# Performance work log

Measured on AMD Instinct MI355X. Metric: run time of the kernel, lower is better.

The kernel has to match this reference:

```python
import jax, jax.numpy as jnp
import numpy as np

N_HEAD = 16
D_HEAD = 64
D_LATENT = 32
BLOCK_SIZE = 2048


def rope_cache(dim, max_seq_len, theta=10000.0):
    inv_freq = 1.0 / (theta ** (jnp.arange(0, dim, 2, dtype=jnp.float32) / dim))
    t = jnp.arange(max_seq_len, dtype=jnp.float32)
    freqs = jnp.einsum('i,j->ij', t, inv_freq)        # [T, dim/2]
    emb = jnp.concatenate([freqs, freqs], axis=-1)    # [T, dim]
    return jnp.cos(emb), jnp.sin(emb)


def apply_rope(x, cos, sin):
    # x: [B, H, T, C]; interleaved-pair rotation as in the torch module
    B, H, T, C = x.shape
    c = cos[:T][None, None]
    s = sin[:T][None, None]
    x1 = x[..., 0::2]
    x2 = x[..., 1::2]
    rotated = jnp.stack((-x2, x1), axis=-1).reshape(B, H, T, C)
    return x * c + rotated * s


def setup_inputs() -> dict:
    key = jax.random.key(0)
    ks = jax.random.split(key, 7)
    sd = 0.02
    return {
        'x':   jax.random.normal(ks[0], (2, 2048, 1024), dtype=jnp.float32),
        'Wq':  jax.random.normal(ks[1], (1024, 1024), dtype=jnp.float32) * sd,
        'Wk':  jax.random.normal(ks[2], (512, 1024), dtype=jnp.float32) * sd,
        'Wv':  jax.random.normal(ks[3], (512, 1024), dtype=jnp.float32) * sd,
        'Wku': jax.random.normal(ks[4], (64, 32), dtype=jnp.float32) * sd,
        'Wvu': jax.random.normal(ks[5], (64, 32), dtype=jnp.float32) * sd,
        'Wc':  jax.random.normal(ks[6], (1024, 1024), dtype=jnp.float32) * sd,
    }


def reference(x, Wq, Wk, Wv, Wku, Wvu, Wc):
    B, T, C = x.shape
    H, Dh, Dl = N_HEAD, D_HEAD, D_LATENT

    # latent KV (compressed cache entries)
    k_lat = (x @ Wk.T).reshape(B, T, H, Dl)   # [B,T,H,Dl]
    v_lat = (x @ Wv.T).reshape(B, T, H, Dl)

    # q and up-projected k/v -> [B,H,T,Dh]
    q = (x @ Wq.T).reshape(B, T, H, Dh).transpose(0, 2, 1, 3)
    k = jnp.einsum('bthl,dl->bhtd', k_lat, Wku)
    v = jnp.einsum('bthl,dl->bhtd', v_lat, Wvu)

    cos, sin = rope_cache(Dh, BLOCK_SIZE)
    q = apply_rope(q, cos, sin)
    k = apply_rope(k, cos, sin)

    scale = 1.0 / jnp.sqrt(jnp.asarray(Dh, dtype=x.dtype))
    att = jnp.einsum('bhqd,bhkd->bhqk', q, k) * scale   # [B,H,T,T]
    causal = jnp.tril(jnp.ones((T, T), dtype=bool))
    att = jnp.where(causal[None, None], att, -jnp.inf)
    att = jax.nn.softmax(att, axis=-1)

    y = jnp.einsum('bhqk,bhkd->bhqd', att, v)           # [B,H,T,Dh]
    y = y.transpose(0, 2, 1, 3).reshape(B, T, C) @ Wc.T  # [B,T,C]
    return y, k_lat, v_lat
```

## Files before the change

### kernel.cpp

```cpp
#include <hip/hip_runtime.h>
#include <math.h>

#define NHEAD  16
#define DHEAD  64
#define DLAT   32
#define TSEQ   2048
#define NBATCH 2
#define CDIM   1024
#define MROWS  (NBATCH*TSEQ)

typedef __attribute__((ext_vector_type(8))) short bf16x8;
typedef __attribute__((ext_vector_type(4))) float f32x4;

#define AS1 __attribute__((address_space(1)))
#define AS3 __attribute__((address_space(3)))

__device__ __forceinline__ unsigned short f2bf(float f) {
    union { float f; unsigned u; } v; v.f = f;
    unsigned r = v.u + 0x7fff + ((v.u >> 16) & 1);
    return (unsigned short)(r >> 16);
}

__device__ __forceinline__ unsigned pk2(float lo, float hi) {
    return (unsigned)f2bf(lo) | ((unsigned)f2bf(hi) << 16);
}

__device__ __forceinline__ unsigned pack_trunc(float hi, float lo) {
    return __builtin_amdgcn_perm(__float_as_uint(hi), __float_as_uint(lo), 0x07060302u);
}

__device__ __forceinline__ void gld_lds16(const unsigned short* g, unsigned short* l) {
    __builtin_amdgcn_global_load_lds((const AS1 void*)g, (AS3 void*)l, 16, 0, 0);
}

__global__ __launch_bounds__(256) void cvt_all(
        const float* __restrict__ x,  const float* __restrict__ wq,
        const float* __restrict__ wk, const float* __restrict__ wv,
        const float* __restrict__ wc, const float* __restrict__ wku,
        const float* __restrict__ wvu,
        unsigned short* __restrict__ xb, unsigned short* __restrict__ wall) {
    int i = (blockIdx.x * 256 + threadIdx.x) * 4;
    const float* src; unsigned short* dst; int off;
    if      (i < 4194304) { src = x;   dst = xb;             off = 0;       }
    else if (i < 5242880) { src = wq;  dst = wall;           off = 4194304; }
    else if (i < 5767168) { src = wk;  dst = wall + 1048576; off = 5242880; }
    else if (i < 6291456) { src = wv;  dst = wall + 1572864; off = 5767168; }
    else if (i < 7340032) { src = wc;  dst = wall + 2097152; off = 6291456; }
    else if (i < 7342080) { src = wku; dst = wall + 3145728; off = 7340032; }
    else                  { src = wvu; dst = wall + 3147776; off = 7342080; }
    float4 v = *(const float4*)(src + (i - off));
    ushort4 o = { f2bf(v.x), f2bf(v.y), f2bf(v.z), f2bf(v.w) };
    *(ushort4*)(dst + (i - off)) = o;
}

__device__ __forceinline__ void gemm_core(
        const unsigned short* __restrict__ A, const unsigned short* __restrict__ W,
        int K, int bm, int bn, unsigned short* As, unsigned short* Bs,
        f32x4 (&acc)[4][4]) {
    const int tid = threadIdx.x;
    const int w = tid >> 6, lane = tid & 63;
    const int quad = lane >> 4, l16 = lane & 15;
    const int wm = (w >> 1) * 64, wn = (w & 1) * 64;

    const int lr = lane >> 2;
    const int le = (lane & 3) * 8;
    const unsigned short* Ag0 = A + (size_t)(bm + w*32 + lr) * K + le;
    const unsigned short* Wg0 = W + (size_t)(bn + w*32 + lr) * K + le;
    unsigned short* AsD0 = &As[(w*32 +  0) * 32];
    unsigned short* AsD1 = &As[(w*32 + 16) * 32];
    unsigned short* BsD0 = &Bs[(w*32 +  0) * 32];
    unsigned short* BsD1 = &Bs[(w*32 + 16) * 32];

    for (int k0 = 0; k0 < K; k0 += 32) {
        gld_lds16(Ag0 + k0,                AsD0);
        gld_lds16(Ag0 + k0 + (size_t)16*K, AsD1);
        gld_lds16(Wg0 + k0,                BsD0);
        gld_lds16(Wg0 + k0 + (size_t)16*K, BsD1);
        __syncthreads();
        bf16x8 af[4], bf[4];
        #pragma unroll
        for (int t = 0; t < 4; ++t)
            af[t] = *(const bf16x8*)&As[(wm + t*16 + l16)*32 + quad*8];
        #pragma unroll
        for (int c = 0; c < 4; ++c)
            bf[c] = *(const bf16x8*)&Bs[(wn + c*16 + l16)*32 + quad*8];
        #pragma unroll
        for (int t = 0; t < 4; ++t)
            #pragma unroll
            for (int c = 0; c < 4; ++c)
                acc[t][c] = __builtin_amdgcn_mfma_f32_16x16x32_bf16(af[t], bf[c], acc[t][c], 0, 0, 0);
        __syncthreads();
    }
}

__global__ __launch_bounds__(256) void gemm_proj(
        const unsigned short* __restrict__ A, const unsigned short* __restrict__ W,
        float* __restrict__ qproj, float* __restrict__ okl, float* __restrict__ ovl,
        int K) {
    __shared__ unsigned short As[128*32];
    __shared__ unsigned short Bs[128*32];
    const int bm = blockIdx.y * 128, bn = blockIdx.x * 128;
    f32x4 acc[4][4] = {};
    gemm_core(A, W, K, bm, bn, As, Bs, acc);

    const int tid = threadIdx.x;
    const int w = tid >> 6, lane = tid & 63;
    const int quad = lane >> 4, l16 = lane & 15;
    const int wm = (w >> 1) * 64, wn = (w & 1) * 64;

    float* base; int ldo;
    if (bn < 1024)      { base = qproj + bn;        ldo = 1024; }
    else if (bn < 1536) { base = okl + (bn - 1024); ldo = 512;  }
    else                { base = ovl + (bn - 1536); ldo = 512;  }

    #pragma unroll
    for (int t = 0; t < 4; ++t)
        #pragma unroll
        for (int c = 0; c < 4; ++c)
            #pragma unroll
            for (int r = 0; r < 4; ++r) {
                int row = bm + wm + t*16 + quad*4 + r;
                int col = wn + c*16 + l16;
                base[(size_t)row * ldo + col] = acc[t][c][r];
            }
}

__global__ __launch_bounds__(256) void gemm_out(
        const unsigned short* __restrict__ A, const unsigned short* __restrict__ W,
        float* __restrict__ O, int N, int K) {
    __shared__ unsigned short As[128*32];
    __shared__ unsigned short Bs[128*32];
    const int bm = blockIdx.y * 128, bn = blockIdx.x * 128;
    f32x4 acc[4][4] = {};
    gemm_core(A, W, K, bm, bn, As, Bs, acc);

    const int tid = threadIdx.x;
    const int w = tid >> 6, lane = tid & 63;
    const int quad = lane >> 4, l16 = lane & 15;
    const int wm = (w >> 1) * 64, wn = (w & 1) * 64;
    #pragma unroll
    for (int t = 0; t < 4; ++t)
        #pragma unroll
        for (int c = 0; c < 4; ++c)
            #pragma unroll
            for (int r = 0; r < 4; ++r) {
                int row = bm + wm + t*16 + quad*4 + r;
                int col = bn + wn + c*16 + l16;
                O[(size_t)row * N + col] = acc[t][c][r];
            }
}

__global__ __launch_bounds__(256) void latup(
        const float* __restrict__ qproj, const float* __restrict__ klat,
        const float* __restrict__ vlat,
        const unsigned short* __restrict__ wkub, const unsigned short* __restrict__ wvub,
        unsigned short* __restrict__ qb, unsigned short* __restrict__ kb,
        unsigned short* __restrict__ vt) {
    __shared__ __attribute__((aligned(16))) unsigned short ksh[4][16][72];
    __shared__ __attribute__((aligned(16))) unsigned short qsh[4][16][72];
    __shared__ __attribute__((aligned(16))) unsigned short vsh[4][64][24];

    const int bh = blockIdx.y, b = bh >> 4, h = bh & 15;
    const int tid = threadIdx.x, w = tid >> 6, lane = tid & 63;
    const int quad = lane >> 4, l16 = lane & 15;
    const int tw = blockIdx.x * 64 + w * 16;
    const int t  = tw + l16;

    const float* klp = klat + ((size_t)(b*TSEQ + t))*(NHEAD*DLAT) + h*DLAT + quad*8;
    const float* vlp = vlat + ((size_t)(b*TSEQ + t))*(NHEAD*DLAT) + h*DLAT + quad*8;
    float4 kA = *(const float4*)klp, kB = *(const float4*)(klp + 4);
    float4 vA = *(const float4*)vlp, vB = *(const float4*)(vlp + 4);

    bf16x8 xk[4], xv[4];
    #pragma unroll
    for (int c = 0; c < 4; ++c) {
        xk[c] = *(const bf16x8*)&wkub[(c*16 + l16)*DLAT + quad*8];
        xv[c] = *(const bf16x8*)&wvub[(c*16 + l16)*DLAT + quad*8];
    }

    union { bf16x8 v; unsigned u[4]; } yk, yv;
    yk.u[0] = pk2(kA.x, kA.y); yk.u[1] = pk2(kA.z, kA.w);
    yk.u[2] = pk2(kB.x, kB.y); yk.u[3] = pk2(kB.z, kB.w);
    yv.u[0] = pk2(vA.x, vA.y); yv.u[1] = pk2(vA.z, vA.w);
    yv.u[2] = pk2(vB.x, vB.y); yv.u[3] = pk2(vB.z, vB.w);

    f32x4 aK[4], aV[4];
    #pragma unroll
    for (int c = 0; c < 4; ++c) {
        f32x4 z = {0.f, 0.f, 0.f, 0.f};
        aK[c] = __builtin_amdgcn_mfma_f32_16x16x32_bf16(xk[c], yk.v, z, 0, 0, 0);
        aV[c] = __builtin_amdgcn_mfma_f32_16x16x32_bf16(xv[c], yv.v, z, 0, 0, 0);
    }

    float C0[4], S0[4], C1[4], S1[4];
    const float tf = (float)t;
    #pragma unroll
    for (int j = 0; j < 4; ++j) {
        float f0 = (float)(quad*4 + j);
        __sincosf(tf * __expf(-f0 * 0.28782313662425572f),          &S0[j], &C0[j]);
        __sincosf(tf * __expf(-(f0 + 16.f) * 0.28782313662425572f), &S1[j], &C1[j]);
    }

    const float* qrow = qproj + ((size_t)(b*TSEQ + t))*CDIM + h*DHEAD;
    #pragma unroll
    for (int c = 0; c < 4; ++c) {
        const float* Cs = (c & 1) ? C1 : C0;
        const float* Ss = (c & 1) ? S1 : S0;
        float a0 = aK[c][0], a1 = aK[c][1], a2 = aK[c][2], a3 = aK[c][3];
        unsigned kw0 = pk2(a0*Cs[0] - a1*Ss[0], a1*Cs[1] + a0*Ss[1]);
        unsigned kw1 = pk2(a2*Cs[2] - a3*Ss[2], a3*Cs[3] + a2*Ss[3]);
        *(uint2*)&ksh[w][l16][c*16 + quad*4] = make_uint2(kw0, kw1);

        float4 qv = *(const float4*)(qrow + c*16 + quad*4);
        unsigned qw0 = pk2((qv.x*Cs[0] - qv.y*Ss[0])*0.125f, (qv.y*Cs[1] + qv.x*Ss[1])*0.125f);
        unsigned qw1 = pk2((qv.z*Cs[2] - qv.w*Ss[2])*0.125f, (qv.w*Cs[3] + qv.z*Ss[3])*0.125f);
        *(uint2*)&qsh[w][l16][c*16 + quad*4] = make_uint2(qw0, qw1);

        vsh[w][c*16 + quad*4 + 0][l16] = f2bf(aV[c][0]);
        vsh[w][c*16 + quad*4 + 1][l16] = f2bf(aV[c][1]);
        vsh[w][c*16 + quad*4 + 2][l16] = f2bf(aV[c][2]);
        vsh[w][c*16 + quad*4 + 3][l16] = f2bf(aV[c][3]);
    }

    __asm__ __volatile__("s_waitcnt lgkmcnt(0)" ::: "memory");

    const int ro = lane >> 2, co = (lane & 3) * 16;
    size_t go = ((size_t)bh*TSEQ + tw + ro)*DHEAD + co;
    int4 k0o = *(const int4*)&ksh[w][ro][co];
    int4 k1o = *(const int4*)&ksh[w][ro][co + 8];
    *(int4*)&kb[go]     = k0o;
    *(int4*)&kb[go + 8] = k1o;
    int4 q0o = *(const int4*)&qsh[w][ro][co];
    int4 q1o = *(const int4*)&qsh[w][ro][co + 8];
    *(int4*)&qb[go]     = q0o;
    *(int4*)&qb[go + 8] = q1o;

    size_t vo = ((size_t)bh*DHEAD + lane)*TSEQ + tw;
    int4 v0o = *(const int4*)&vsh[w][lane][0];
    int4 v1o = *(const int4*)&vsh[w][lane][8];
    *(int4*)&vt[vo]     = v0o;
    *(int4*)&vt[vo + 8] = v1o;
}

__global__ __launch_bounds__(256, 2) void flash_attn(
        const unsigned short* __restrict__ qb, const unsigned short* __restrict__ kb,
        const unsigned short* __restrict__ vtb, unsigned short* __restrict__ yatt) {
    const int bh = blockIdx.x;
    const int b = bh >> 4, h = bh & 15;

    __shared__ unsigned short Ks[2][128][64];
    __shared__ unsigned short VTs[2][64][128];

    const int tid  = threadIdx.x;
    const int wq   = tid >> 6;
    const int lane = tid & 63;
    const int quad = lane >> 4;
    const int l16  = lane & 15;

    const unsigned short* Kbase = kb  + (size_t)bh * TSEQ * DHEAD;
    const unsigned short* Vbase = vtb + (size_t)bh * DHEAD * TSEQ;

    const int kr8 = lane >> 3, kcp = lane & 7;
    const int kcl = (kcp ^ kr8) * 8;
    const int vr4 = lane >> 4, vcp = lane & 15;

    const int kx0 = (quad ^ (l16 & 7)) * 8;
    const int kx1 = ((quad + 4) ^ (l16 & 7)) * 8;

    const int idx01 = (((lane >> 4) & 1) * 32 + l16) * 4;
    const int idx23 = idx01 + 64;
    const bool hi = (lane & 32) != 0;

    for (int half = 0; half < 2; ++half) {
        const int qt = half ? (31 - (int)blockIdx.y) : (int)blockIdx.y;
        const int n128 = (qt + 2) >> 1;

        const unsigned short* qbase =
            qb + ((size_t)bh*TSEQ + qt*64 + wq*16 + l16) * DHEAD + quad*8;
        bf16x8 qB0 = *(const bf16x8*)qbase;
        bf16x8 qB1 = *(const bf16x8*)(qbase + 32);

        f32x4 oacc[4] = {};
        float m_run = -1e30f, l_run = 0.f;

        __syncthreads();
        #pragma unroll
        for (int i = 0; i < 4; ++i) {
            gld_lds16(Kbase + (size_t)(wq*32 + i*8 + kr8)*DHEAD + kcl,
                      &Ks[0][wq*32 + i*8][0]);
            int vcl = (vcp ^ ((i*4 + vr4) & 15)) * 8;
            gld_lds16(Vbase + (size_t)(wq*16 + i*4 + vr4)*TSEQ + vcl,
                      &VTs[0][wq*16 + i*4][0]);
        }
        __syncthreads();

        for (int j = 0; j < n128; ++j) {
            const int buf = j & 1;
            if (j + 1 < n128) {
                const int kc = (j + 1) * 128;
                #pragma unroll
                for (int i = 0; i < 4; ++i) {
                    gld_lds16(Kbase + (size_t)(kc + wq*32 + i*8 + kr8)*DHEAD + kcl,
                              &Ks[buf^1][wq*32 + i*8][0]);
                    int vcl = (vcp ^ ((i*4 + vr4) & 15)) * 8;
                    gld_lds16(Vbase + (size_t)(wq*16 + i*4 + vr4)*TSEQ + kc + vcl,
                              &VTs[buf^1][wq*16 + i*4][0]);
                }
            }

            f32x4 sacc[8];
            #pragma unroll
            for (int c = 0; c < 8; ++c) {
                bf16x8 ak0 = *(const bf16x8*)&Ks[buf][c*16 + l16][kx0];
                bf16x8 ak1 = *(const bf16x8*)&Ks[buf][c*16 + l16][kx1];
                f32x4 z = {0.f, 0.f, 0.f, 0.f};
                z = __builtin_amdgcn_mfma_f32_16x16x32_bf16(ak0, qB0, z, 0, 0, 0);
                z = __builtin_amdgcn_mfma_f32_16x16x32_bf16(ak1, qB1, z, 0, 0, 0);
                sacc[c] = z;
            }
            if (j == n128 - 1) {
                #pragma unroll
                for (int c = 0; c < 8; ++c)
                    #pragma unroll
                    for (int r = 0; r < 4; ++r)
                        if (j*128 + c*16 + quad*4 + r > qt*64 + wq*16 + l16)
                            sacc[c][r] = -1e30f;
            }

            float mx = -1e30f;
            #pragma unroll
            for (int c = 0; c < 8; ++c)
                #pragma unroll
                for (int r = 0; r < 4; ++r) mx = fmaxf(mx, sacc[c][r]);
            mx = fmaxf(mx, __shfl_xor(mx, 16, 64));
            mx = fmaxf(mx, __shfl_xor(mx, 32, 64));
            float mn = fmaxf(m_run, mx);
            float alpha = __expf(m_run - mn);
            m_run = mn;
            float ls = 0.f;
            #pragma unroll
            for (int c = 0; c < 8; ++c)
                #pragma unroll
                for (int r = 0; r < 4; ++r) {
                    float p = __expf(sacc[c][r] - mn);
                    sacc[c][r] = p;
                    ls += p;
                }
            ls += __shfl_xor(ls, 16, 64);
            ls += __shfl_xor(ls, 32, 64);
            l_run = l_run * alpha + ls;
            #pragma unroll
            for (int c = 0; c < 4; ++c)
                #pragma unroll
                for (int r = 0; r < 4; ++r) oacc[c][r] *= alpha;

            #pragma unroll
            for (int g = 0; g < 4; ++g) {
                unsigned p0a = pack_trunc(sacc[2*g][1],   sacc[2*g][0]);
                unsigned p0b = pack_trunc(sacc[2*g][3],   sacc[2*g][2]);
                unsigned p1a = pack_trunc(sacc[2*g+1][1], sacc[2*g+1][0]);
                unsigned p1b = pack_trunc(sacc[2*g+1][3], sacc[2*g+1][2]);
                union { bf16x8 v; int d[4]; } bP;
                int a0 = __builtin_amdgcn_ds_bpermute(idx01, (int)p0a);
                int b0 = __builtin_amdgcn_ds_bpermute(idx01, (int)p1a);
                bP.d[0] = hi ? b0 : a0;
                int a1 = __builtin_amdgcn_ds_bpermute(idx01, (int)p0b);
                int b1 = __builtin_amdgcn_ds_bpermute(idx01, (int)p1b);
                bP.d[1] = hi ? b1 : a1;
                int a2 = __builtin_amdgcn_ds_bpermute(idx23, (int)p0a);
                int b2 = __builtin_amdgcn_ds_bpermute(idx23, (int)p1a);
                bP.d[2] = hi ? b2 : a2;
                int a3 = __builtin_amdgcn_ds_bpermute(idx23, (int)p0b);
                int b3 = __builtin_amdgcn_ds_bpermute(idx23, (int)p1b);
                bP.d[3] = hi ? b3 : a3;
                #pragma unroll
                for (int c = 0; c < 4; ++c) {
                    bf16x8 av = *(const bf16x8*)&VTs[buf][c*16 + l16][((g*4 + quad) ^ l16) * 8];
                    oacc[c] = __builtin_amdgcn_mfma_f32_16x16x32_bf16(av, bP.v, oacc[c], 0, 0, 0);
                }
            }

            __syncthreads();
        }

        float invl = 1.0f / l_run;
        unsigned short* Wt = &Ks[0][0][0] + wq * (16*72);
        #pragma unroll
        for (int c = 0; c < 4; ++c)
            #pragma unroll
            for (int r = 0; r < 4; ++r)
                Wt[(size_t)l16*72 + c*16 + quad*4 + r] = f2bf(oacc[c][r] * invl);
        __asm__ __volatile__("" ::: "memory");
        #pragma unroll
        for (int p = 0; p < 2; ++p) {
            int row = p*8 + (lane >> 3);
            int d0 = (lane & 7) * 8;
            int4 val = *(const int4*)&Wt[row*72 + d0];
            int tg = qt*64 + wq*16 + row;
            *(int4*)&yatt[((size_t)(b*TSEQ + tg))*CDIM + h*DHEAD + d0] = val;
        }
    }
}

extern "C" void kernel_launch(void* const* d_in, const int* in_sizes, int n_in,
                              void* d_out, int out_size, void* d_ws, size_t ws_size,
                              hipStream_t stream) {
    const float* x   = (const float*)d_in[0];
    const float* Wq  = (const float*)d_in[1];
    const float* Wk  = (const float*)d_in[2];
    const float* Wv  = (const float*)d_in[3];
    const float* Wku = (const float*)d_in[4];
    const float* Wvu = (const float*)d_in[5];
    const float* Wc  = (const float*)d_in[6];

    float* out_y  = (float*)d_out;
    float* out_kl = out_y  + (size_t)MROWS * CDIM;
    float* out_vl = out_kl + (size_t)MROWS * NHEAD*DLAT;

    float* qproj = (float*)d_ws;
    unsigned short* xb   = (unsigned short*)(qproj + (size_t)MROWS*CDIM);
    unsigned short* qb   = xb  + (size_t)MROWS*CDIM;
    unsigned short* kb   = qb  + (size_t)MROWS*CDIM;
    unsigned short* vt   = kb  + (size_t)MROWS*CDIM;
    unsigned short* wall = vt  + (size_t)MROWS*CDIM;
    unsigned short* wcb  = wall + (size_t)2048*CDIM;
    unsigned short* wkub = wall + 3145728;
    unsigned short* wvub = wall + 3147776;
    unsigned short* yatt = (unsigned short*)qproj;

    cvt_all<<<7172, 256, 0, stream>>>(x, Wq, Wk, Wv, Wc, Wku, Wvu, xb, wall);

    gemm_proj<<<dim3(2048/128, MROWS/128), 256, 0, stream>>>(
        xb, wall, qproj, out_kl, out_vl, CDIM);

    latup<<<dim3(TSEQ/64, NBATCH*NHEAD), 256, 0, stream>>>(
        qproj, out_kl, out_vl, wkub, wvub, qb, kb, vt);

    flash_attn<<<dim3(NBATCH*NHEAD, 16), 256, 0, stream>>>(qb, kb, vt, yatt);

    gemm_out<<<dim3(CDIM/128, MROWS/128), 256, 0, stream>>>(yatt, wcb, out_y, CDIM, CDIM);
}
```

Baseline: 204.3 us.

## Use exp2 softmax with lazy rescaling and 16x16x16 MFMA for PV

Folds log2(e) into the Q scale so the softmax uses exp2 directly, and skips the running-max rescale of the output accumulator unless the new max exceeds the old by more than 8. It replaces the ds_bpermute-based P reshuffle with 16x16x16 bf16 MFMAs that consume P straight from the score accumulator layout, reading V with 4-element loads. It also raises wave priority around the MFMA blocks. The lazy rescale lets probabilities grow up to 2^8 before renormalizing, which trades a little bf16 precision headroom for fewer multiplies, and the PV step now issues twice as many smaller MFMAs.

```diff
diff --git a/kernel.cpp b/kernel.cpp
--- a/kernel.cpp
+++ b/kernel.cpp
@@ -10,6 +10,7 @@
 #define MROWS  (NBATCH*TSEQ)
 
 typedef __attribute__((ext_vector_type(8))) short bf16x8;
+typedef __attribute__((ext_vector_type(4))) short bf16x4;
 typedef __attribute__((ext_vector_type(4))) float f32x4;
 
 #define AS1 __attribute__((address_space(1)))
@@ -31,6 +32,16 @@
 
 __device__ __forceinline__ void gld_lds16(const unsigned short* g, unsigned short* l) {
     __builtin_amdgcn_global_load_lds((const AS1 void*)g, (AS3 void*)l, 16, 0, 0);
+}
+
+__device__ __forceinline__ f32x4 mfma_16x16x16_bf16(bf16x4 a, bf16x4 b, f32x4 c) {
+#if __has_builtin(__builtin_amdgcn_mfma_f32_16x16x16bf16_1k)
+    return __builtin_amdgcn_mfma_f32_16x16x16bf16_1k(a, b, c, 0, 0, 0);
+#else
+    asm volatile("v_mfma_f32_16x16x16_bf16 %0, %1, %2, %0\n\ts_nop 4"
+                 : "+v"(c) : "v"(a), "v"(b));
+    return c;
+#endif
 }
 
 __global__ __launch_bounds__(256) void cvt_all(
@@ -150,6 +161,7 @@
             }
 }
 
+#define QSCALE 0.18033688011112042f
 __global__ __launch_bounds__(256) void latup(
         const float* __restrict__ qproj, const float* __restrict__ klat,
         const float* __restrict__ vlat,
@@ -212,8 +224,8 @@
         *(uint2*)&ksh[w][l16][c*16 + quad*4] = make_uint2(kw0, kw1);
 
         float4 qv = *(const float4*)(qrow + c*16 + quad*4);
-        unsigned qw0 = pk2((qv.x*Cs[0] - qv.y*Ss[0])*0.125f, (qv.y*Cs[1] + qv.x*Ss[1])*0.125f);
-        unsigned qw1 = pk2((qv.z*Cs[2] - qv.w*Ss[2])*0.125f, (qv.w*Cs[3] + qv.z*Ss[3])*0.125f);
+        unsigned qw0 = pk2((qv.x*Cs[0] - qv.y*Ss[0])*QSCALE, (qv.y*Cs[1] + qv.x*Ss[1])*QSCALE);
+        unsigned qw1 = pk2((qv.z*Cs[2] - qv.w*Ss[2])*QSCALE, (qv.w*Cs[3] + qv.z*Ss[3])*QSCALE);
         *(uint2*)&qsh[w][l16][c*16 + quad*4] = make_uint2(qw0, qw1);
 
         vsh[w][c*16 + quad*4 + 0][l16] = f2bf(aV[c][0]);
@@ -266,10 +278,7 @@
 
     const int kx0 = (quad ^ (l16 & 7)) * 8;
     const int kx1 = ((quad + 4) ^ (l16 & 7)) * 8;
-
-    const int idx01 = (((lane >> 4) & 1) * 32 + l16) * 4;
-    const int idx23 = idx01 + 64;
-    const bool hi = (lane & 32) != 0;
+    const int vq = (quad >> 1), vodd = (quad & 1) * 4;
 
     for (int half = 0; half < 2; ++half) {
         const int qt = half ? (31 - (int)blockIdx.y) : (int)blockIdx.y;
@@ -309,6 +318,7 @@
             }
 
             f32x4 sacc[8];
+            __builtin_amdgcn_s_setprio(1);
             #pragma unroll
             for (int c = 0; c < 8; ++c) {
                 bf16x8 ak0 = *(const bf16x8*)&Ks[buf][c*16 + l16][kx0];
@@ -318,6 +328,7 @@
                 z = __builtin_amdgcn_mfma_f32_16x16x32_bf16(ak1, qB1, z, 0, 0, 0);
                 sacc[c] = z;
             }
+            __builtin_amdgcn_s_setprio(0);
             if (j == n128 - 1) {
                 #pragma unroll
                 for (int c = 0; c < 8; ++c)
@@ -334,51 +345,43 @@
                 for (int r = 0; r < 4; ++r) mx = fmaxf(mx, sacc[c][r]);
             mx = fmaxf(mx, __shfl_xor(mx, 16, 64));
             mx = fmaxf(mx, __shfl_xor(mx, 32, 64));
-            float mn = fmaxf(m_run, mx);
-            float alpha = __expf(m_run - mn);
-            m_run = mn;
+            if (!__all(mx <= m_run + 8.f)) {
+                float mn = fmaxf(m_run, mx);
+                float alpha = __builtin_exp2f(m_run - mn);
+                m_run = mn;
+                l_run *= alpha;
+                #pragma unroll
+                for (int c = 0; c < 4; ++c)
+                    #pragma unroll
+                    for (int r = 0; r < 4; ++r) oacc[c][r] *= alpha;
+            }
             float ls = 0.f;
             #pragma unroll
             for (int c = 0; c < 8; ++c)
                 #pragma unroll
                 for (int r = 0; r < 4; ++r) {
-                    float p = __expf(sacc[c][r] - mn);
+                    float p = __builtin_exp2f(sacc[c][r] - m_run);
                     sacc[c][r] = p;
                     ls += p;
                 }
             ls += __shfl_xor(ls, 16, 64);
             ls += __shfl_xor(ls, 32, 64);
-            l_run = l_run * alpha + ls;
-            #pragma unroll
-            for (int c = 0; c < 4; ++c)
-                #pragma unroll
-                for (int r = 0; r < 4; ++r) oacc[c][r] *= alpha;
-
-            #pragma unroll
-            for (int g = 0; g < 4; ++g) {
-                unsigned p0a = pack_trunc(sacc[2*g][1],   sacc[2*g][0]);
-                unsigned p0b = pack_trunc(sacc[2*g][3],   sacc[2*g][2]);
-                unsigned p1a = pack_trunc(sacc[2*g+1][1], sacc[2*g+1][0]);
-                unsigned p1b = pack_trunc(sacc[2*g+1][3], sacc[2*g+1][2]);
-                union { bf16x8 v; int d[4]; } bP;
-                int a0 = __builtin_amdgcn_ds_bpermute(idx01, (int)p0a);
-                int b0 = __builtin_amdgcn_ds_bpermute(idx01, (int)p1a);
-                bP.d[0] = hi ? b0 : a0;
-                int a1 = __builtin_amdgcn_ds_bpermute(idx01, (int)p0b);
-                int b1 = __builtin_amdgcn_ds_bpermute(idx01, (int)p1b);
-                bP.d[1] = hi ? b1 : a1;
-                int a2 = __builtin_amdgcn_ds_bpermute(idx23, (int)p0a);
-                int b2 = __builtin_amdgcn_ds_bpermute(idx23, (int)p1a);
-                bP.d[2] = hi ? b2 : a2;
-                int a3 = __builtin_amdgcn_ds_bpermute(idx23, (int)p0b);
-                int b3 = __builtin_amdgcn_ds_bpermute(idx23, (int)p1b);
-                bP.d[3] = hi ? b3 : a3;
-                #pragma unroll
-                for (int c = 0; c < 4; ++c) {
-                    bf16x8 av = *(const bf16x8*)&VTs[buf][c*16 + l16][((g*4 + quad) ^ l16) * 8];
-                    oacc[c] = __builtin_amdgcn_mfma_f32_16x16x32_bf16(av, bP.v, oacc[c], 0, 0, 0);
+            l_run += ls;
+
+            __builtin_amdgcn_s_setprio(1);
+            #pragma unroll
+            for (int c = 0; c < 8; ++c) {
+                union { bf16x4 v; unsigned u[2]; } bP;
+                bP.u[0] = pack_trunc(sacc[c][1], sacc[c][0]);
+                bP.u[1] = pack_trunc(sacc[c][3], sacc[c][2]);
+                const int vcol = ((2*c + vq) ^ l16) * 8 + vodd;
+                #pragma unroll
+                for (int dc = 0; dc < 4; ++dc) {
+                    bf16x4 av = *(const bf16x4*)&VTs[buf][dc*16 + l16][vcol];
+                    oacc[dc] = mfma_16x16x16_bf16(av, bP.v, oacc[dc]);
                 }
             }
+            __builtin_amdgcn_s_setprio(0);
 
             __syncthreads();
         }
```

New measurement: 206.9 us. Within noise of the previous version (+1.3%).
